# Optimization experiments

Hardware: AMD Instinct MI355X
Metric: run time of the kernel (lower is better)

The kernel has to match this reference:

```python
import jax, jax.numpy as jnp
import numpy as np

B, S, D = 8, 4096, 1024
M, K, R = 32, 3, 64
RAD = 8      # anchor_radius
KS = 3       # causal pool kernel
LN_EPS = 1e-5


def layernorm(x, g, b):
    mu = jnp.mean(x, axis=-1, keepdims=True)
    var = jnp.mean((x - mu) ** 2, axis=-1, keepdims=True)
    return (x - mu) * jax.lax.rsqrt(var + LN_EPS) * g + b


def l2norm(v, eps=1e-6):
    return v / jnp.maximum(jnp.linalg.norm(v, axis=-1, keepdims=True), eps)


def causal_pool(x, k):
    # replicate-pad front, sliding mean of width k (stride 1) via cumsum
    if k <= 1:
        return x
    xp = jnp.pad(x, ((0, 0), (k - 1, 0), (0, 0)), mode='edge')
    cs = jnp.cumsum(xp, axis=1)
    cs = jnp.pad(cs, ((0, 0), (1, 0), (0, 0)))
    return (cs[:, k:, :] - cs[:, :-k, :]) / k


def setup_inputs() -> dict:
    key = jax.random.key(0)
    ks = jax.random.split(key, 16)
    f32 = jnp.float32
    return {
        'pt_hidden': jax.random.normal(ks[0], (B, S, D), f32),
        'ts_hidden': jax.random.normal(ks[1], (B, S, D), f32),
        'patch_positions': jnp.arange(S, dtype=f32),
        'mode_centroids': jax.random.normal(ks[2], (M, D), f32),
        'stability_gate': jax.random.uniform(ks[3], (B, S, 1), f32),
        # P2TAdapter params
        'anchor_w': jax.random.normal(ks[4], (D,), f32) / np.sqrt(D),
        'anchor_b': jnp.zeros((), f32),
        'trans_a': jax.random.normal(ks[5], (M, D, R), f32) * 0.01,
        'trans_b': jax.random.normal(ks[6], (M, D, R), f32) * 0.01,
        'out_norm_g': jnp.ones((D,), f32),
        'out_norm_b': jnp.zeros((D,), f32),
        # AntiCollapseSelectiveBridge params
        'ts_norm_g': jnp.ones((D,), f32),
        'ts_norm_b': jnp.zeros((D,), f32),
        'pt_norm_g': jnp.ones((D,), f32),
        'pt_norm_b': jnp.zeros((D,), f32),
        'shared_W': jax.random.normal(ks[7], (2 * D + 1, D), f32) * 0.01,
        'shared_b': jnp.zeros((D,), f32),
        'ts_up_W': jax.random.normal(ks[8], (D, D), f32) * 0.006,
        'pt_up_W': jax.random.normal(ks[9], (D, D), f32) * 0.006,
        'bridge_scale': jnp.asarray(0.24, f32),
    }


def reference(pt_hidden, ts_hidden, patch_positions, mode_centroids, stability_gate,
              anchor_w, anchor_b, trans_a, trans_b, out_norm_g, out_norm_b,
              ts_norm_g, ts_norm_b, pt_norm_g, pt_norm_b,
              shared_W, shared_b, ts_up_W, pt_up_W, bridge_scale):
    # ---------------- P2TAdapter ----------------
    scores = jnp.einsum('bsd,d->bs', pt_hidden, anchor_w) + anchor_b        # [B,S]
    topk_scores, anchor_idx = jax.lax.top_k(scores, K)                      # [B,K]
    anchor_vectors = jnp.take_along_axis(pt_hidden, anchor_idx[..., None], axis=1)  # [B,K,D]

    basis_logits = jnp.einsum('bkd,md->bkm', l2norm(anchor_vectors), l2norm(mode_centroids))
    basis_w = jax.nn.softmax(basis_logits, axis=-1)                         # [B,K,M]
    dyn_a = jnp.einsum('bkm,mdr->bkdr', basis_w, trans_a)
    dyn_b = jnp.einsum('bkm,mdr->bkdr', basis_w, trans_b)
    low = jnp.einsum('bkd,bkdr->bkr', anchor_vectors, dyn_a)
    translated = jnp.einsum('bkr,bkdr->bkd', low, dyn_b)                    # [B,K,D]

    # neighborhood spread weights around anchors
    anchor_pos = patch_positions[anchor_idx]                                # [B,K]
    dist = jnp.abs(patch_positions[None, None, :] - anchor_pos[..., None])  # [B,K,S]
    nmask = (dist <= float(RAD)).astype(pt_hidden.dtype)
    logits = jnp.where(nmask == 0, -10000.0, -dist / float(RAD))
    spread_w = jax.nn.softmax(logits, axis=-1)                              # [B,K,S]

    anchor_update = jnp.einsum('bks,bkd->bsd', spread_w, translated)        # [B,S,D]
    ts_aug = layernorm(ts_hidden + anchor_update, out_norm_g, out_norm_b)

    # ---------------- AntiCollapseSelectiveBridge ----------------
    tsn = layernorm(ts_aug, ts_norm_g, ts_norm_b)
    ptn = layernorm(pt_hidden, pt_norm_g, pt_norm_b)
    eps = 1e-6
    dot = jnp.sum(tsn * ptn, axis=-1)
    cos = dot / (jnp.maximum(jnp.linalg.norm(tsn, axis=-1), eps) *
                 jnp.maximum(jnp.linalg.norm(ptn, axis=-1), eps))
    agreement = 0.5 * (1.0 + cos)[..., None]                                # [B,S,1]
    z = (agreement - 0.72) / 0.2
    focus = 0.2 + 0.8 * jnp.exp(-0.5 * z * z)
    bridge_gate = agreement * focus * stability_gate                        # curriculum_factor = 1

    shared = jnp.concatenate([tsn, ptn, bridge_gate], axis=-1) @ shared_W + shared_b
    shared = causal_pool(shared, KS)
    blend = jax.nn.sigmoid(bridge_scale) * 0.35
    lb = blend * bridge_gate                                                # [B,S,1]
    ts_out = ts_aug + lb * ((shared - tsn) @ ts_up_W)
    pt_out = pt_hidden + lb * ((shared - ptn) @ pt_up_W)
    return (ts_out, pt_out)
```

## Files before the change

### kernel.cpp

```cpp
#include <hip/hip_runtime.h>

#define Bn 8
#define Sn 4096
#define Dn 1024
#define Mn 32
#define Kk 3
#define Rn 64
#define BSn (Bn*Sn)
#define NBK (Bn*Kk)

typedef unsigned short u16;
typedef short short8 __attribute__((ext_vector_type(8)));
typedef float f32x4 __attribute__((ext_vector_type(4)));

__device__ __forceinline__ u16 f2bf(float f){
  unsigned u = __builtin_bit_cast(unsigned, f);
  u += 0x7fffu + ((u >> 16) & 1u);
  return (u16)(u >> 16);
}
__device__ __forceinline__ float bf2f(u16 h){
  unsigned u = ((unsigned)h) << 16;
  return __builtin_bit_cast(float, u);
}

__device__ __forceinline__ void cp16(const void* g, void* l){
  __builtin_amdgcn_global_load_lds(
      (const __attribute__((address_space(1))) void*)g,
      (__attribute__((address_space(3))) void*)l, 16, 0, 0);
}

__device__ __forceinline__ float2 block_sum2(float a, float b, float* red){
  #pragma unroll
  for (int off = 32; off > 0; off >>= 1){
    a += __shfl_down(a, off, 64);
    b += __shfl_down(b, off, 64);
  }
  int lane = threadIdx.x & 63, w = threadIdx.x >> 6;
  if (lane == 0){ red[w] = a; red[4+w] = b; }
  __syncthreads();
  float2 r;
  r.x = red[0]+red[1]+red[2]+red[3];
  r.y = red[4]+red[5]+red[6]+red[7];
  __syncthreads();
  return r;
}

__device__ __forceinline__ float3 block_sum3(float a, float b, float c, float* red){
  #pragma unroll
  for (int off = 32; off > 0; off >>= 1){
    a += __shfl_down(a, off, 64);
    b += __shfl_down(b, off, 64);
    c += __shfl_down(c, off, 64);
  }
  int lane = threadIdx.x & 63, w = threadIdx.x >> 6;
  if (lane == 0){ red[w] = a; red[4+w] = b; red[8+w] = c; }
  __syncthreads();
  float3 r;
  r.x = red[0]+red[1]+red[2]+red[3];
  r.y = red[4]+red[5]+red[6]+red[7];
  r.z = red[8]+red[9]+red[10]+red[11];
  __syncthreads();
  return r;
}

__global__ __launch_bounds__(256) void k_scores(const float* __restrict__ pt,
    const float* __restrict__ aw, const float* __restrict__ ab, float* __restrict__ scores){
  int lane = threadIdx.x & 63, w = threadIdx.x >> 6;
  int row = blockIdx.x * 4 + w;
  const float4* x  = (const float4*)(pt + (size_t)row * Dn);
  const float4* wv = (const float4*)aw;
  float acc = 0.f;
  #pragma unroll
  for (int c = 0; c < 4; c++){
    int i = c * 64 + lane;
    float4 a = x[i], b = wv[i];
    acc += a.x*b.x + a.y*b.y + a.z*b.z + a.w*b.w;
  }
  #pragma unroll
  for (int off = 32; off > 0; off >>= 1) acc += __shfl_down(acc, off, 64);
  if (lane == 0) scores[row] = acc + ab[0];
}

__global__ __launch_bounds__(256) void k_top3(const float* __restrict__ scores, int* __restrict__ aidx){
  __shared__ float tv[256*3];
  __shared__ int   ti[256*3];
  int b = blockIdx.x, t = threadIdx.x;
  float v[3] = {-1e38f, -1e38f, -1e38f};
  int  id[3] = {0x7fffffff, 0x7fffffff, 0x7fffffff};
  for (int s = t; s < Sn; s += 256){
    float sc = scores[b*Sn + s];
    if (sc > v[0] || (sc == v[0] && s < id[0])){ v[2]=v[1]; id[2]=id[1]; v[1]=v[0]; id[1]=id[0]; v[0]=sc; id[0]=s; }
    else if (sc > v[1] || (sc == v[1] && s < id[1])){ v[2]=v[1]; id[2]=id[1]; v[1]=sc; id[1]=s; }
    else if (sc > v[2] || (sc == v[2] && s < id[2])){ v[2]=sc; id[2]=s; }
  }
  for (int j = 0; j < 3; j++){ tv[t*3+j] = v[j]; ti[t*3+j] = id[j]; }
  __syncthreads();
  if (t == 0){
    float bv[3] = {-1e38f, -1e38f, -1e38f};
    int   bi[3] = {0x7fffffff, 0x7fffffff, 0x7fffffff};
    for (int c = 0; c < 256*3; c++){
      float sc = tv[c]; int ii = ti[c];
      if (sc > bv[0] || (sc == bv[0] && ii < bi[0])){ bv[2]=bv[1]; bi[2]=bi[1]; bv[1]=bv[0]; bi[1]=bi[0]; bv[0]=sc; bi[0]=ii; }
      else if (sc > bv[1] || (sc == bv[1] && ii < bi[1])){ bv[2]=bv[1]; bi[2]=bi[1]; bv[1]=sc; bi[1]=ii; }
      else if (sc > bv[2] || (sc == bv[2] && ii < bi[2])){ bv[2]=sc; bi[2]=ii; }
    }
    for (int j = 0; j < 3; j++) aidx[b*3+j] = bi[j];
  }
}

__global__ __launch_bounds__(256) void k_adapter_w(const float* __restrict__ pt,
    const float* __restrict__ cent, const float* __restrict__ pp, const int* __restrict__ aidx,
    float* __restrict__ A24, float* __restrict__ gw, float* __restrict__ invZ){
  __shared__ float a_lds[Dn];
  __shared__ float logitv[Mn];
  __shared__ float red[12];
  int bk = blockIdx.x; int b = bk / Kk;
  int t = threadIdx.x;
  int p = aidx[bk];
  const float* arow = pt + ((size_t)b*Sn + p) * Dn;
  for (int d = t; d < Dn; d += 256){ float v = arow[d]; a_lds[d] = v; A24[(size_t)bk*Dn + d] = v; }
  __syncthreads();
  float ss = 0.f;
  for (int d = t; d < Dn; d += 256){ float v = a_lds[d]; ss += v*v; }
  float2 rr0 = block_sum2(ss, 0.f, red);
  float na = fmaxf(sqrtf(rr0.x), 1e-6f);
  int lane = t & 63, w = t >> 6;
  for (int mi = 0; mi < 8; mi++){
    int m = w*8 + mi;
    const float* c = cent + (size_t)m * Dn;
    float dt = 0.f, cs = 0.f;
    for (int d = lane; d < Dn; d += 64){ float cv = c[d]; dt += a_lds[d]*cv; cs += cv*cv; }
    #pragma unroll
    for (int off = 32; off > 0; off >>= 1){ dt += __shfl_down(dt, off, 64); cs += __shfl_down(cs, off, 64); }
    if (lane == 0){ float nc = fmaxf(sqrtf(cs), 1e-6f); logitv[m] = dt / (na * nc); }
  }
  __syncthreads();
  if (t == 0){
    float mx = -1e30f;
    for (int m = 0; m < Mn; m++) mx = fmaxf(mx, logitv[m]);
    float sm = 0.f, e[Mn];
    for (int m = 0; m < Mn; m++){ e[m] = expf(logitv[m]-mx); sm += e[m]; }
    float inv = 1.f / sm;
    for (int m = 0; m < Mn; m++) gw[bk*Mn + m] = e[m] * inv;
  }
  {
    float zp = 0.f; float ppp = pp[p];
    for (int s2 = t; s2 < Sn; s2 += 256){
      float dd = fabsf(pp[s2] - ppp);
      if (dd <= 8.0f) zp += expf(-dd * 0.125f);
    }
    float2 zr = block_sum2(zp, 0.f, red);
    if (t == 0) invZ[bk] = 1.f / zr.x;
  }
}

__global__ __launch_bounds__(256) void k_lowpart(const float* __restrict__ ta,
    const float* __restrict__ A24, float* __restrict__ part_low){
  __shared__ float ta_s[64*64];
  __shared__ float a_s[NBK*64];
  int dc = blockIdx.x, m = blockIdx.y;
  int t = threadIdx.x;
  int d0 = dc * 64;
  const float4* src = (const float4*)(ta + ((size_t)m*Dn + d0) * Rn);
  float4* dst = (float4*)ta_s;
  #pragma unroll
  for (int c = 0; c < 4; c++) dst[t + c*256] = src[t + c*256];
  for (int idx = t; idx < NBK*64; idx += 256){
    int bk = idx >> 6, dl = idx & 63;
    a_s[idx] = A24[(size_t)bk*Dn + d0 + dl];
  }
  __syncthreads();
  int r = t & 63, g = t >> 6;
  #pragma unroll
  for (int j = 0; j < 6; j++){
    int bk = g*6 + j;
    float acc = 0.f;
    #pragma unroll 8
    for (int d = 0; d < 64; d++) acc += a_s[bk*64 + d] * ta_s[d*64 + r];
    part_low[(((size_t)bk*Mn + m)*16 + dc)*64 + r] = acc;
  }
}

__global__ __launch_bounds__(64) void k_lowfin(const float* __restrict__ part_low,
    const float* __restrict__ gw, float* __restrict__ lowb){
  int bk = blockIdx.x, r = threadIdx.x;
  float acc = 0.f;
  for (int m = 0; m < Mn; m++){
    float s = 0.f;
    #pragma unroll
    for (int dc = 0; dc < 16; dc++)
      s += part_low[(((size_t)bk*Mn + m)*16 + dc)*64 + r];
    acc += gw[bk*Mn + m] * s;
  }
  lowb[bk*64 + r] = acc;
}

__global__ __launch_bounds__(256) void k_transpart(const float* __restrict__ tb,
    const float* __restrict__ lowb, float* __restrict__ transp){
  __shared__ float tb_t[64*65];
  __shared__ float low_s[NBK*64];
  int dc = blockIdx.x, m = blockIdx.y;
  int t = threadIdx.x;
  int d0 = dc * 64;
  const float* src = tb + ((size_t)m*Dn + d0) * Rn;
  for (int idx = t; idx < 4096; idx += 256){
    int d = idx >> 6, r = idx & 63;
    tb_t[r*65 + d] = src[idx];
  }
  for (int idx = t; idx < NBK*64; idx += 256) low_s[idx] = lowb[idx];
  __syncthreads();
  int dl = t & 63, g = t >> 6;
  #pragma unroll
  for (int j = 0; j < 6; j++){
    int bk = g*6 + j;
    float acc = 0.f;
    #pragma unroll 8
    for (int r = 0; r < 64; r++) acc += tb_t[r*65 + dl] * low_s[bk*64 + r];
    transp[((size_t)bk*Mn + m)*Dn + d0 + dl] = acc;
  }
}

__global__ __launch_bounds__(256) void k_transfin(const float* __restrict__ transp,
    const float* __restrict__ gw, float* __restrict__ transl){
  int bk = blockIdx.x, t = threadIdx.x;
  for (int d = t; d < Dn; d += 256){
    float acc = 0.f;
    #pragma unroll 8
    for (int m = 0; m < Mn; m++)
      acc += gw[bk*Mn + m] * transp[((size_t)bk*Mn + m)*Dn + d];
    transl[(size_t)bk*Dn + d] = acc;
  }
}

__global__ __launch_bounds__(256) void k_transpose(const float* __restrict__ src,
    u16* __restrict__ dst, int Ks){
  __shared__ float tile[32][33];
  int kb = blockIdx.x * 32, nb = blockIdx.y * 32;
  int tx = threadIdx.x & 31, ty = threadIdx.x >> 5;
  #pragma unroll
  for (int r = 0; r < 32; r += 8)
    tile[ty+r][tx] = src[(size_t)(kb+ty+r) * Dn + nb + tx];
  __syncthreads();
  #pragma unroll
  for (int r = 0; r < 32; r += 8)
    dst[(size_t)(nb+ty+r) * Ks + kb + tx] = f2bf(tile[tx][ty+r]);
}

__global__ __launch_bounds__(256) void k_rows(
    const float* __restrict__ ts, const float* __restrict__ pt,
    const float* __restrict__ stab, const float* __restrict__ transl,
    const int* __restrict__ aidx, const float* __restrict__ invZ,
    const float* __restrict__ pp,
    const float* __restrict__ og, const float* __restrict__ ob,
    const float* __restrict__ tgp, const float* __restrict__ tbp,
    const float* __restrict__ pgp, const float* __restrict__ pbp,
    float* __restrict__ ts_aug_out, u16* __restrict__ Xcat, float* __restrict__ gate){
  __shared__ float red[12];
  int row = blockIdx.x; int b = row >> 12; int s = row & 4095;
  int t = threadIdx.x;
  size_t base = (size_t)row * Dn;
  const float4 xin = *(const float4*)(ts + base + 4*t);
  float x0 = xin.x, x1 = xin.y, x2 = xin.z, x3 = xin.w;
  float pps = pp[s];
  for (int k = 0; k < Kk; k++){
    int p = aidx[b*Kk + k];
    float dd = fabsf(pps - pp[p]);
    if (dd <= 8.0f){
      float coef = expf(-dd * 0.125f) * invZ[b*Kk + k];
      const float4 tr = *(const float4*)(transl + ((size_t)(b*Kk + k)) * Dn + 4*t);
      x0 += coef*tr.x; x1 += coef*tr.y; x2 += coef*tr.z; x3 += coef*tr.w;
    }
  }
  float2 r = block_sum2(x0+x1+x2+x3, x0*x0+x1*x1+x2*x2+x3*x3, red);
  float mu = r.x * (1.f/Dn); float var = r.y * (1.f/Dn) - mu*mu;
  float rs = 1.f / sqrtf(var + 1e-5f);
  float4 g4 = *(const float4*)(og + 4*t), b4 = *(const float4*)(ob + 4*t);
  float a0 = (x0-mu)*rs*g4.x + b4.x;
  float a1 = (x1-mu)*rs*g4.y + b4.y;
  float a2 = (x2-mu)*rs*g4.z + b4.z;
  float a3 = (x3-mu)*rs*g4.w + b4.w;
  float4 sto; sto.x=a0; sto.y=a1; sto.z=a2; sto.w=a3;
  *(float4*)(ts_aug_out + base + 4*t) = sto;
  r = block_sum2(a0+a1+a2+a3, a0*a0+a1*a1+a2*a2+a3*a3, red);
  mu = r.x * (1.f/Dn); var = r.y * (1.f/Dn) - mu*mu;
  rs = 1.f / sqrtf(var + 1e-5f);
  g4 = *(const float4*)(tgp + 4*t); b4 = *(const float4*)(tbp + 4*t);
  float t0 = (a0-mu)*rs*g4.x + b4.x;
  float t1 = (a1-mu)*rs*g4.y + b4.y;
  float t2 = (a2-mu)*rs*g4.z + b4.z;
  float t3 = (a3-mu)*rs*g4.w + b4.w;
  const float4 pv = *(const float4*)(pt + base + 4*t);
  r = block_sum2(pv.x+pv.y+pv.z+pv.w, pv.x*pv.x+pv.y*pv.y+pv.z*pv.z+pv.w*pv.w, red);
  mu = r.x * (1.f/Dn); var = r.y * (1.f/Dn) - mu*mu;
  rs = 1.f / sqrtf(var + 1e-5f);
  g4 = *(const float4*)(pgp + 4*t); b4 = *(const float4*)(pbp + 4*t);
  float p0 = (pv.x-mu)*rs*g4.x + b4.x;
  float p1 = (pv.y-mu)*rs*g4.y + b4.y;
  float p2 = (pv.z-mu)*rs*g4.z + b4.z;
  float p3 = (pv.w-mu)*rs*g4.w + b4.w;
  ushort4 pk;
  pk.x = f2bf(t0); pk.y = f2bf(t1); pk.z = f2bf(t2); pk.w = f2bf(t3);
  *(ushort4*)(Xcat + (size_t)row*2048 + 4*t) = pk;
  pk.x = f2bf(p0); pk.y = f2bf(p1); pk.z = f2bf(p2); pk.w = f2bf(p3);
  *(ushort4*)(Xcat + (size_t)row*2048 + Dn + 4*t) = pk;
  float3 rr = block_sum3(t0*p0+t1*p1+t2*p2+t3*p3,
                         t0*t0+t1*t1+t2*t2+t3*t3,
                         p0*p0+p1*p1+p2*p2+p3*p3, red);
  if (t == 0){
    float cosv = rr.x / (fmaxf(sqrtf(rr.y), 1e-6f) * fmaxf(sqrtf(rr.z), 1e-6f));
    float ag = 0.5f * (1.f + cosv);
    float z = (ag - 0.72f) * 5.f;
    float focus = 0.2f + 0.8f * expf(-0.5f*z*z);
    gate[row] = ag * focus * stab[row];
  }
}

__global__ __launch_bounds__(512, 2) void k_gemm(
    const u16* __restrict__ A, const u16* __restrict__ Bt, int K, int mode,
    float* __restrict__ out0, const float* __restrict__ sbias, const float* __restrict__ Wlast,
    const float* __restrict__ gate, float* __restrict__ dts,
    const float* __restrict__ ptin, float* __restrict__ dpt, const float* __restrict__ bscale){
  __shared__ __attribute__((aligned(16))) char smem[131072];
  const int NT = K >> 6;
  const int tid = threadIdx.x;
  const int lane = tid & 63, w = tid >> 6;
  const int wm = w >> 2, wn = w & 3;
  const int r15 = lane & 15, quad = lane >> 4;
  const int bid = blockIdx.x;
  const int bm = (bid & 7) * 16 + ((bid >> 3) & 15);
  const int bn = bid >> 7;
  const int m0 = bm * 256, n0 = bn * 256;

  const int row0 = tid >> 3, j0 = tid & 7;
  const int js = j0 ^ (row0 & 7);
  const size_t rowbytes = (size_t)K * 2;
  const char* gA = (const char*)A + (size_t)(m0 + row0) * rowbytes + js * 16;
  const char* gB = (const char*)Bt + (size_t)(n0 + row0) * rowbytes + js * 16;
  const size_t rstep64 = rowbytes << 6;
  char* lA = smem + tid * 16;
  char* lB = smem + 65536 + tid * 16;

  auto stgA = [&](int half, int tile, int buf){
    const char* s = gA + (size_t)half * (rstep64 << 1) + (size_t)tile * 128;
    char* d = lA + buf * 32768 + half * 16384;
    cp16(s, d); cp16(s + rstep64, d + 8192);
  };
  auto stgB = [&](int half, int tile, int buf){
    const char* s = gB + (size_t)half * (rstep64 << 1) + (size_t)tile * 128;
    char* d = lB + buf * 32768 + half * 16384;
    cp16(s, d); cp16(s + rstep64, d + 8192);
  };

  int aoff[4][2], boff[2][2];
  #pragma unroll
  for (int fi = 0; fi < 4; fi++){
    int rl = wm*64 + fi*16 + r15;
    #pragma unroll
    for (int ks = 0; ks < 2; ks++)
      aoff[fi][ks] = rl*128 + ((((ks<<2) + quad) ^ (r15 & 7)) << 4);
  }
  #pragma unroll
  for (int fj = 0; fj < 2; fj++){
    int rn = wn*32 + fj*16 + r15;
    #pragma unroll
    for (int ks = 0; ks < 2; ks++)
      boff[fj][ks] = rn*128 + ((((ks<<2) + quad) ^ (r15 & 7)) << 4);
  }

  short8 ar[4][2];
  short8 br[2][2][2];
  f32x4 acc[8][4];
  #pragma unroll
  for (int i = 0; i < 8; i++)
    #pragma unroll
    for (int j = 0; j < 4; j++){ f32x4 z = {0.f,0.f,0.f,0.f}; acc[i][j] = z; }

  auto rdA = [&](int ph, int buf){
    #pragma unroll
    for (int fi = 0; fi < 4; fi++)
      #pragma unroll
      for (int ks = 0; ks < 2; ks++)
        ar[fi][ks] = *(const short8*)(smem + buf*32768 + ph*16384 + aoff[fi][ks]);
  };
  auto rdB = [&](int p, int buf){
    #pragma unroll
    for (int fj = 0; fj < 2; fj++)
      #pragma unroll
      for (int ks = 0; ks < 2; ks++)
        br[p][fj][ks] = *(const short8*)(smem + 65536 + buf*32768 + p*16384 + boff[fj][ks]);
  };
  auto mma16 = [&](int ap, int bp){
    __builtin_amdgcn_s_barrier();
    asm volatile("s_waitcnt lgkmcnt(0)" ::: "memory");
    __builtin_amdgcn_sched_barrier(0);
    __builtin_amdgcn_s_setprio(1);
    #pragma unroll
    for (int fi = 0; fi < 4; fi++)
      #pragma unroll
      for (int fj = 0; fj < 2; fj++)
        #pragma unroll
        for (int ks = 0; ks < 2; ks++)
          acc[ap*4+fi][bp*2+fj] = __builtin_amdgcn_mfma_f32_16x16x32_bf16(
              ar[fi][ks], br[bp][fj][ks], acc[ap*4+fi][bp*2+fj], 0, 0, 0);
    __builtin_amdgcn_s_setprio(0);
  };

  stgA(0, 0, 0); stgA(1, 0, 0); stgB(0, 0, 0); stgB(1, 0, 0);
  stgA(0, 1, 1); stgB(1, 1, 1);
  asm volatile("s_waitcnt vmcnt(4)" ::: "memory");
  __builtin_amdgcn_s_barrier();

  auto tileStep = [&](int t, int buf){
    rdA(0, buf); rdB(0, buf);
    if (t+1 < NT) stgA(1, t+1, buf^1);
    mma16(0, 0);
    __builtin_amdgcn_s_barrier();
    rdB(1, buf);
    if (t+1 < NT) stgB(0, t+1, buf^1);
    mma16(0, 1);
    __builtin_amdgcn_s_barrier();
    rdA(1, buf);
    if (t+2 < NT) stgA(0, t+2, buf);
    mma16(1, 1);
    __builtin_amdgcn_s_barrier();
    if (t+2 < NT) stgB(1, t+2, buf);
    mma16(1, 0);
    if (t+2 < NT){ asm volatile("s_waitcnt vmcnt(4)" ::: "memory"); }
    else         { asm volatile("s_waitcnt vmcnt(0)" ::: "memory"); }
    __builtin_amdgcn_s_barrier();
  };
  for (int t = 0; t < NT; t += 2){ tileStep(t, 0); tileStep(t+1, 1); }

  float blend = 0.f;
  if (mode != 0) blend = 0.35f / (1.f + expf(-bscale[0]));
  #pragma unroll
  for (int mi = 0; mi < 8; mi++){
    int rowb = m0 + (mi>>2)*128 + wm*64 + (mi&3)*16 + quad*4;
    #pragma unroll
    for (int nj = 0; nj < 4; nj++){
      int col = n0 + (nj>>1)*128 + wn*32 + (nj&1)*16 + r15;
      #pragma unroll
      for (int rg = 0; rg < 4; rg++){
        int rw = rowb + rg;
        size_t idx = (size_t)rw * Dn + col;
        float v = acc[mi][nj][rg];
        if (mode == 0){
          out0[idx] = v + sbias[col] + gate[rw] * Wlast[col];
        } else if (mode == 1){
          dts[idx] = dts[idx] + blend * gate[rw] * v;
        } else {
          dpt[idx] = ptin[idx] + blend * gate[rw] * v;
        }
      }
    }
  }
}

__global__ __launch_bounds__(256) void k_pooldiff(const float* __restrict__ sh,
    const u16* __restrict__ Xcat, u16* __restrict__ Xts, u16* __restrict__ Xpt){
  int row = blockIdx.x; int s = row & 4095; int t = threadIdx.x;
  size_t base = (size_t)row * Dn + 4*t;
  int rm1 = (s >= 1) ? row-1 : row;
  int rm2 = (s >= 2) ? row-2 : rm1;
  float4 a = *(const float4*)(sh + base);
  float4 b = *(const float4*)(sh + (size_t)rm1*Dn + 4*t);
  float4 c = *(const float4*)(sh + (size_t)rm2*Dn + 4*t);
  float p0 = (a.x+b.x+c.x)*(1.f/3.f);
  float p1 = (a.y+b.y+c.y)*(1.f/3.f);
  float p2 = (a.z+b.z+c.z)*(1.f/3.f);
  float p3 = (a.w+b.w+c.w)*(1.f/3.f);
  ushort4 tn = *(const ushort4*)(Xcat + (size_t)row*2048 + 4*t);
  ushort4 pn = *(const ushort4*)(Xcat + (size_t)row*2048 + Dn + 4*t);
  ushort4 o;
  o.x = f2bf(p0 - bf2f(tn.x)); o.y = f2bf(p1 - bf2f(tn.y));
  o.z = f2bf(p2 - bf2f(tn.z)); o.w = f2bf(p3 - bf2f(tn.w));
  *(ushort4*)(Xts + base) = o;
  o.x = f2bf(p0 - bf2f(pn.x)); o.y = f2bf(p1 - bf2f(pn.y));
  o.z = f2bf(p2 - bf2f(pn.z)); o.w = f2bf(p3 - bf2f(pn.w));
  *(ushort4*)(Xpt + base) = o;
}

extern "C" void kernel_launch(void* const* d_in, const int* in_sizes, int n_in,
                              void* d_out, int out_size, void* d_ws, size_t ws_size,
                              hipStream_t stream){
  const float* pt   = (const float*)d_in[0];
  const float* ts   = (const float*)d_in[1];
  const float* pp   = (const float*)d_in[2];
  const float* cent = (const float*)d_in[3];
  const float* stab = (const float*)d_in[4];
  const float* aw   = (const float*)d_in[5];
  const float* ab   = (const float*)d_in[6];
  const float* ta   = (const float*)d_in[7];
  const float* tb   = (const float*)d_in[8];
  const float* og   = (const float*)d_in[9];
  const float* ob   = (const float*)d_in[10];
  const float* tg   = (const float*)d_in[11];
  const float* tbn  = (const float*)d_in[12];
  const float* pg   = (const float*)d_in[13];
  const float* pb   = (const float*)d_in[14];
  const float* sW   = (const float*)d_in[15];
  const float* sb   = (const float*)d_in[16];
  const float* tsW  = (const float*)d_in[17];
  const float* ptW  = (const float*)d_in[18];
  const float* bsc  = (const float*)d_in[19];
  float* out_ts = (float*)d_out;
  float* out_pt = out_ts + (size_t)BSn * Dn;

  char* wbase = (char*)d_ws; size_t off = 0;
  auto alloc = [&](size_t bytes) -> void* {
    void* p = wbase + off;
    off += (bytes + 255) & ~(size_t)255;
    return p;
  };
  float* scores  = (float*)alloc((size_t)BSn * 4);
  int*   aidx    = (int*)  alloc(256);
  float* invZ    = (float*)alloc(256);
  float* transl  = (float*)alloc((size_t)NBK*Dn * 4);
  float* gate    = (float*)alloc((size_t)BSn * 4);
  float* A24     = (float*)alloc((size_t)NBK*Dn * 4);
  float* gw      = (float*)alloc((size_t)NBK*Mn * 4);
  float* part_low= (float*)alloc((size_t)NBK*Mn*16*64 * 4);
  float* lowb    = (float*)alloc((size_t)NBK*64 * 4);
  float* transp  = (float*)alloc((size_t)NBK*Mn*Dn * 4);
  u16*   Xcat    = (u16*)  alloc((size_t)BSn * 2048 * 2);
  float* shmem   = (float*)alloc((size_t)BSn * Dn * 4);
  u16*   Xts     = (u16*)  alloc((size_t)BSn * Dn * 2);
  u16*   Xpt     = (u16*)  alloc((size_t)BSn * Dn * 2);
  u16*   WtS     = (u16*)  alloc((size_t)Dn * 2048 * 2);
  u16*   WtT     = (u16*)  alloc((size_t)Dn * Dn * 2);
  u16*   WtP     = (u16*)  alloc((size_t)Dn * Dn * 2);

  k_scores<<<BSn/4, 256, 0, stream>>>(pt, aw, ab, scores);
  k_top3<<<Bn, 256, 0, stream>>>(scores, aidx);
  k_adapter_w<<<NBK, 256, 0, stream>>>(pt, cent, pp, aidx, A24, gw, invZ);
  k_lowpart<<<dim3(16, Mn), 256, 0, stream>>>(ta, A24, part_low);
  k_lowfin<<<NBK, 64, 0, stream>>>(part_low, gw, lowb);
  k_transpart<<<dim3(16, Mn), 256, 0, stream>>>(tb, lowb, transp);
  k_transfin<<<NBK, 256, 0, stream>>>(transp, gw, transl);
  k_transpose<<<dim3(64,32), 256, 0, stream>>>(sW, WtS, 2048);
  k_transpose<<<dim3(32,32), 256, 0, stream>>>(tsW, WtT, 1024);
  k_transpose<<<dim3(32,32), 256, 0, stream>>>(ptW, WtP, 1024);
  k_rows<<<BSn, 256, 0, stream>>>(ts, pt, stab, transl, aidx, invZ, pp,
                                  og, ob, tg, tbn, pg, pb, out_ts, Xcat, gate);
  k_gemm<<<512, 512, 0, stream>>>(Xcat, WtS, 2048, 0,
      shmem, sb, sW + (size_t)2048*Dn, gate, nullptr, nullptr, nullptr, bsc);
  k_pooldiff<<<BSn, 256, 0, stream>>>(shmem, Xcat, Xts, Xpt);
  k_gemm<<<512, 512, 0, stream>>>(Xts, WtT, 1024, 1,
      nullptr, nullptr, nullptr, gate, out_ts, nullptr, nullptr, bsc);
  k_gemm<<<512, 512, 0, stream>>>(Xpt, WtP, 1024, 2,
      nullptr, nullptr, nullptr, gate, nullptr, pt, out_pt, bsc);
}
```

Measured before the change: 1.444 ms.

## Stage GEMM epilogue through LDS for coalesced float4 stores and reorder prefetches

The GEMM epilogue now writes accumulator fragments into swizzled shared memory and then reads back full rows, so each lane issues coalesced float4 global loads and stores for the bias/gate fusion and read-modify-write paths. Previously each thread wrote scattered scalar elements. The main loop also swaps the order of the A/B next-tile staging and adds intermediate vmcnt waits to adjust load/compute overlap. This adds LDS round trips and extra barriers in the epilogue, and the relaxed wait counts must still match the number of outstanding loads.

Measured after the change: 1.310 ms. 1.1x faster.

```diff
diff --git a/kernel.cpp b/kernel.cpp
--- a/kernel.cpp
+++ b/kernel.cpp
@@ -412,12 +412,13 @@
 
   auto tileStep = [&](int t, int buf){
     rdA(0, buf); rdB(0, buf);
+    if (t+1 < NT) stgB(0, t+1, buf^1);
+    mma16(0, 0);
+    __builtin_amdgcn_s_barrier();
+    rdB(1, buf);
     if (t+1 < NT) stgA(1, t+1, buf^1);
-    mma16(0, 0);
-    __builtin_amdgcn_s_barrier();
-    rdB(1, buf);
-    if (t+1 < NT) stgB(0, t+1, buf^1);
     mma16(0, 1);
+    asm volatile("s_waitcnt vmcnt(8)" ::: "memory");
     __builtin_amdgcn_s_barrier();
     rdA(1, buf);
     if (t+2 < NT) stgA(0, t+2, buf);
@@ -425,7 +426,7 @@
     __builtin_amdgcn_s_barrier();
     if (t+2 < NT) stgB(1, t+2, buf);
     mma16(1, 0);
-    if (t+2 < NT){ asm volatile("s_waitcnt vmcnt(4)" ::: "memory"); }
+    if (t+2 < NT){ asm volatile("s_waitcnt vmcnt(6)" ::: "memory"); }
     else         { asm volatile("s_waitcnt vmcnt(0)" ::: "memory"); }
     __builtin_amdgcn_s_barrier();
   };
@@ -433,24 +434,53 @@
 
   float blend = 0.f;
   if (mode != 0) blend = 0.35f / (1.f + expf(-bscale[0]));
-  #pragma unroll
-  for (int mi = 0; mi < 8; mi++){
-    int rowb = m0 + (mi>>2)*128 + wm*64 + (mi&3)*16 + quad*4;
-    #pragma unroll
-    for (int nj = 0; nj < 4; nj++){
-      int col = n0 + (nj>>1)*128 + wn*32 + (nj&1)*16 + r15;
+  float* lC = (float*)smem;
+  const int cols0 = n0 + lane*4;
+  float4 sb4 = {0.f,0.f,0.f,0.f}, wl4 = {0.f,0.f,0.f,0.f};
+  if (mode == 0){
+    sb4 = *(const float4*)(sbias + cols0);
+    wl4 = *(const float4*)(Wlast + cols0);
+  }
+  #pragma unroll
+  for (int c = 0; c < 2; c++){
+    __builtin_amdgcn_s_barrier();
+    #pragma unroll
+    for (int mi2 = 0; mi2 < 4; mi2++){
+      int mi = c*4 + mi2;
+      int lrow = wm*64 + mi2*16 + quad*4;
       #pragma unroll
-      for (int rg = 0; rg < 4; rg++){
-        int rw = rowb + rg;
-        size_t idx = (size_t)rw * Dn + col;
-        float v = acc[mi][nj][rg];
-        if (mode == 0){
-          out0[idx] = v + sbias[col] + gate[rw] * Wlast[col];
-        } else if (mode == 1){
-          dts[idx] = dts[idx] + blend * gate[rw] * v;
-        } else {
-          dpt[idx] = ptin[idx] + blend * gate[rw] * v;
+      for (int nj = 0; nj < 4; nj++){
+        int col = (nj>>1)*128 + wn*32 + (nj&1)*16 + r15;
+        #pragma unroll
+        for (int rg = 0; rg < 4; rg++){
+          int rr = lrow + rg;
+          lC[rr*256 + (col ^ (((rr>>2)&3)<<4))] = acc[mi][nj][rg];
         }
+      }
+    }
+    __builtin_amdgcn_s_barrier();
+    #pragma unroll
+    for (int r = 0; r < 16; r++){
+      int rr = w*16 + r;
+      int grow = m0 + c*128 + rr;
+      float4 v = *(const float4*)(lC + rr*256 + ((lane*4) ^ (((rr>>2)&3)<<4)));
+      size_t gi = (size_t)grow * Dn + cols0;
+      if (mode == 0){
+        float g = gate[grow];
+        float4 o;
+        o.x = v.x + sb4.x + g*wl4.x; o.y = v.y + sb4.y + g*wl4.y;
+        o.z = v.z + sb4.z + g*wl4.z; o.w = v.w + sb4.w + g*wl4.w;
+        *(float4*)(out0 + gi) = o;
+      } else if (mode == 1){
+        float bg = blend * gate[grow];
+        float4 d = *(const float4*)(dts + gi);
+        d.x += bg*v.x; d.y += bg*v.y; d.z += bg*v.z; d.w += bg*v.w;
+        *(float4*)(dts + gi) = d;
+      } else {
+        float bg = blend * gate[grow];
+        float4 p = *(const float4*)(ptin + gi);
+        p.x += bg*v.x; p.y += bg*v.y; p.z += bg*v.z; p.w += bg*v.w;
+        *(float4*)(dpt + gi) = p;
       }
     }
   }
```
